# Kernel tuning notes

Measured on AMD Instinct MI355X. Metric: run time of the kernel, lower is better.

The kernel has to match this reference:

```python
import jax, jax.numpy as jnp
import numpy as np
import math

N_HEADS = 16

def _rope_tables(T, D, dtype):
    # inv_freq over even dims, emb = [freqs, freqs] -> [T, D]
    inv_freq = 1.0 / (10000.0 ** (jnp.arange(0, D, 2, dtype=jnp.float32) / D))
    freqs = jnp.arange(T, dtype=jnp.float32)[:, None] * inv_freq[None, :]  # [T, D/2]
    emb = jnp.concatenate([freqs, freqs], axis=-1)  # [T, D]
    return jnp.cos(emb).astype(dtype), jnp.sin(emb).astype(dtype)

def _rotate_half(x):
    d = x.shape[-1] // 2
    return jnp.concatenate([-x[..., d:], x[..., :d]], axis=-1)

def setup_inputs() -> dict:
    key = jax.random.key(0)
    ks = jax.random.split(key, 5)
    B, T, C = 2, 2048, 1024
    s = 1.0 / math.sqrt(C)
    return {
        "x": jax.random.normal(ks[0], (B, T, C), dtype=jnp.float32),
        "Wq": jax.random.normal(ks[1], (C, C), dtype=jnp.float32) * s,
        "Wk": jax.random.normal(ks[2], (C, C), dtype=jnp.float32) * s,
        "Wv": jax.random.normal(ks[3], (C, C), dtype=jnp.float32) * s,
        "Wo": jax.random.normal(ks[4], (C, C), dtype=jnp.float32) * s,
    }

def reference(x, Wq, Wk, Wv, Wo):
    B, T, C = x.shape
    H = N_HEADS
    D = C // H
    # QKV projections (torch Linear, bias=False: y = x @ W.T), split into heads
    def proj(W):
        return (x @ W.T).reshape(B, T, H, D).transpose(0, 2, 1, 3)  # [B,H,T,D]
    q, k, v = proj(Wq), proj(Wk), proj(Wv)
    # RoPE
    cos, sin = _rope_tables(T, D, x.dtype)  # [T,D] each, broadcast over B,H
    q = q * cos + _rotate_half(q) * sin
    k = k * cos + _rotate_half(k) * sin
    # scaled dot-product attention with causal mask
    scale = 1.0 / math.sqrt(D)
    attn = jnp.einsum('bhtd,bhsd->bhts', q, k) * scale  # [B,H,T,T]
    row = jnp.arange(T)[:, None]
    col = jnp.arange(T)[None, :]
    attn = jnp.where(col > row, -jnp.inf, attn)
    p = jax.nn.softmax(attn, axis=-1)
    out = jnp.einsum('bhts,bhsd->bhtd', p, v)  # [B,H,T,D]
    out = out.transpose(0, 2, 1, 3).reshape(B, T, C)
    return out @ Wo.T
```

## Files before the change

### kernel.cpp

```cpp
#include <hip/hip_runtime.h>
#include <hip/hip_bf16.h>


typedef __hip_bfloat16 bf16;
typedef __attribute__((ext_vector_type(8))) short bf16x8;
typedef __attribute__((ext_vector_type(4))) float f32x4;
typedef __attribute__((ext_vector_type(4))) short short4v;

#define MFMA16(a, b, c) __builtin_amdgcn_mfma_f32_16x16x32_bf16((a), (b), (c), 0, 0, 0)

constexpr int Bn = 2, Hn = 16, Tn = 2048, Dn = 64, Cn = 1024;
constexpr size_t NE = (size_t)Bn * Tn * Cn;
constexpr size_t WE = (size_t)Cn * Cn;
constexpr float QSCALE = 0.125f * 1.44269504088896f;

__device__ inline unsigned short bfbits(float x) {
    bf16 b = __float2bfloat16(x);
    return *(unsigned short*)&b;
}

__device__ inline bf16x8 pack8(f32x4 a, f32x4 b) {
    bf16x8 r;
#pragma unroll
    for (int i = 0; i < 4; ++i) r[i] = (short)bfbits(a[i]);
#pragma unroll
    for (int i = 0; i < 4; ++i) r[4 + i] = (short)bfbits(b[i]);
    return r;
}

__device__ inline void gl_lds16(const bf16* g, unsigned short* l) {
    __builtin_amdgcn_global_load_lds(
        (const __attribute__((address_space(1))) void*)g,
        (__attribute__((address_space(3))) void*)l, 16, 0, 0);
}

__device__ inline void stage64(const bf16* gbase, int ld, unsigned short* lds,
                               int wave, int lane) {
#pragma unroll
    for (int j = 0; j < 2; ++j) {
        int p = j * 256 + wave * 64 + lane;
        int row = p >> 3, ch = (p & 7) ^ (row & 7);
        gl_lds16(gbase + (size_t)row * ld + ch * 8,
                 lds + (size_t)(j * 256 + wave * 64) * 8);
    }
}

__device__ inline bf16x8 ldsfrag(const unsigned short* base, int row, int ch) {
    return *(const bf16x8*)&base[row * 64 + ((ch ^ (row & 7)) * 8)];
}

__global__ __launch_bounds__(256) void convert_kernel(
    const float* __restrict__ x, const float* __restrict__ wq,
    const float* __restrict__ wk, const float* __restrict__ wv,
    const float* __restrict__ wo, bf16* __restrict__ dst)
{
    int blk = blockIdx.x;
    int lane = threadIdx.x & 63;
    int lx = lane & 15, quad = lane >> 4;
    const float* src;
    size_t doff;
    if (blk < 2048) {
        int frag = blk * 4 + (threadIdx.x >> 6);
        int mt = frag >> 5, kc = frag & 31;
        src = x + (size_t)(mt * 16 + lx) * Cn + kc * 32 + quad * 8;
        doff = (size_t)frag * 512 + lane * 8;
    } else {
        int w = (blk - 2048) >> 9, b = (blk - 2048) & 511;
        const float* s4[4] = {wq, wk, wv, wo};
        int frag = b * 4 + (threadIdx.x >> 6);
        int nb = frag >> 5, kc = frag & 31;
        src = s4[w] + (size_t)(nb * 16 + lx) * Cn + kc * 32 + quad * 8;
        doff = NE + (size_t)w * WE + (size_t)frag * 512 + lane * 8;
    }
    f32x4 a = *(const f32x4*)(src);
    f32x4 b2 = *(const f32x4*)(src + 4);
    *(bf16x8*)(dst + doff) = pack8(a, b2);
}

__global__ __launch_bounds__(256) void gemm_qkv_kernel(
    const bf16* __restrict__ Xf, const bf16* __restrict__ Wbase,
    bf16* __restrict__ Qo, bf16* __restrict__ Ko, bf16* __restrict__ Vo)
{
    const int bm = blockIdx.x, bn = blockIdx.y, wsel = blockIdx.z;
    const bf16* W = Wbase + (size_t)wsel * WE;
    const int tid  = threadIdx.x;
    const int wave = tid >> 6, lane = tid & 63;
    const int lx   = lane & 15, quad = lane >> 4;
    const int wm = wave >> 1, wn = wave & 1;

    const int mt0 = bm * 8 + wm * 4;
    const int nb0 = bn * 8 + wn * 4;
    const bf16* afrag = Xf + (size_t)mt0 * 32 * 512 + (size_t)lane * 8;
    const bf16* wfrag = W + (size_t)nb0 * 32 * 512 + (size_t)lane * 8;

    f32x4 acc[4][4] = {};
    bf16x8 acur[4], bcur[4], anxt[4], bnxt[4];
#pragma unroll
    for (int i = 0; i < 4; ++i) {
        acur[i] = *(const bf16x8*)(afrag + (size_t)i * 32 * 512);
        bcur[i] = *(const bf16x8*)(wfrag + (size_t)i * 32 * 512);
    }
    for (int kc = 0; kc < 32; ++kc) {
        if (kc < 31) {
#pragma unroll
            for (int i = 0; i < 4; ++i) {
                anxt[i] = *(const bf16x8*)(afrag + ((size_t)i * 32 + kc + 1) * 512);
                bnxt[i] = *(const bf16x8*)(wfrag + ((size_t)i * 32 + kc + 1) * 512);
            }
        }
#pragma unroll
        for (int mt = 0; mt < 4; ++mt)
#pragma unroll
            for (int nt = 0; nt < 4; ++nt)
                acc[mt][nt] = MFMA16(acur[mt], bcur[nt], acc[mt][nt]);
#pragma unroll
        for (int i = 0; i < 4; ++i) { acur[i] = anxt[i]; bcur[i] = bnxt[i]; }
    }

    const int h = bn * 2 + wn;
    if (wsel <= 1) {
#pragma unroll
        for (int mt = 0; mt < 4; ++mt)
#pragma unroll
            for (int r = 0; r < 4; ++r) {
                int mg = bm * 128 + wm * 64 + mt * 16 + quad * 4 + r;
                int t  = mg & (Tn - 1);
#pragma unroll
                for (int nt = 0; nt < 2; ++nt) {
                    int d = nt * 16 + lx;
                    float ang = (float)t * __expf(-(float)d * 0.2878231366f);
                    float c, s;
                    __sincosf(ang, &s, &c);
                    float a0 = acc[mt][nt][r], a1 = acc[mt][nt + 2][r];
                    acc[mt][nt][r]     = a0 * c - a1 * s;
                    acc[mt][nt + 2][r] = a1 * c + a0 * s;
                }
            }
    }

#pragma unroll
    for (int mt = 0; mt < 4; ++mt) {
        int mg0 = bm * 128 + wm * 64 + mt * 16 + quad * 4;
        int b = mg0 >> 11, t0 = mg0 & (Tn - 1);
        if (wsel == 0) {
#pragma unroll
            for (int nt = 0; nt < 4; ++nt)
#pragma unroll
                for (int r = 0; r < 4; ++r) {
                    int d = nt * 16 + lx;
                    Qo[((size_t)(b * Hn + h) * Tn + t0 + r) * Dn + d] =
                        __float2bfloat16(acc[mt][nt][r] * QSCALE);
                }
        } else if (wsel == 1) {
#pragma unroll
            for (int nt = 0; nt < 4; ++nt)
#pragma unroll
                for (int r = 0; r < 4; ++r) {
                    int d = nt * 16 + lx;
                    Ko[((size_t)(b * Hn + h) * Tn + t0 + r) * Dn + d] =
                        __float2bfloat16(acc[mt][nt][r]);
                }
        } else {
#pragma unroll
            for (int nt = 0; nt < 4; ++nt) {
                int d = nt * 16 + lx;
                short4v pk;
#pragma unroll
                for (int r = 0; r < 4; ++r) pk[r] = (short)bfbits(acc[mt][nt][r]);
                *(short4v*)&Vo[((size_t)(b * Hn + h) * Dn + d) * Tn + t0] = pk;
            }
        }
    }
}

__global__ __launch_bounds__(256) void gemm_out_kernel(
    const bf16* __restrict__ Af, const bf16* __restrict__ W, float* __restrict__ Out)
{
    const int bm = blockIdx.x, bn = blockIdx.y;
    const int tid  = threadIdx.x;
    const int wave = tid >> 6, lane = tid & 63;
    const int lx   = lane & 15, quad = lane >> 4;
    const int wm = wave >> 1, wn = wave & 1;

    const int mt0 = bm * 8 + wm * 4;
    const int nb0 = bn * 4 + wn * 2;
    const bf16* afrag = Af + (size_t)mt0 * 32 * 512 + (size_t)lane * 8;
    const bf16* wfrag = W + (size_t)nb0 * 32 * 512 + (size_t)lane * 8;

    f32x4 acc[4][2] = {};
    bf16x8 acur[4], bcur[2], anxt[4], bnxt[2];
#pragma unroll
    for (int i = 0; i < 4; ++i)
        acur[i] = *(const bf16x8*)(afrag + (size_t)i * 32 * 512);
#pragma unroll
    for (int i = 0; i < 2; ++i)
        bcur[i] = *(const bf16x8*)(wfrag + (size_t)i * 32 * 512);
    for (int kc = 0; kc < 32; ++kc) {
        if (kc < 31) {
#pragma unroll
            for (int i = 0; i < 4; ++i)
                anxt[i] = *(const bf16x8*)(afrag + ((size_t)i * 32 + kc + 1) * 512);
#pragma unroll
            for (int i = 0; i < 2; ++i)
                bnxt[i] = *(const bf16x8*)(wfrag + ((size_t)i * 32 + kc + 1) * 512);
        }
#pragma unroll
        for (int mt = 0; mt < 4; ++mt)
#pragma unroll
            for (int nt = 0; nt < 2; ++nt)
                acc[mt][nt] = MFMA16(acur[mt], bcur[nt], acc[mt][nt]);
#pragma unroll
        for (int i = 0; i < 4; ++i) acur[i] = anxt[i];
#pragma unroll
        for (int i = 0; i < 2; ++i) bcur[i] = bnxt[i];
    }
#pragma unroll
    for (int mt = 0; mt < 4; ++mt)
#pragma unroll
        for (int nt = 0; nt < 2; ++nt)
#pragma unroll
            for (int r = 0; r < 4; ++r) {
                int mg = bm * 128 + wm * 64 + mt * 16 + quad * 4 + r;
                int ng = bn * 64 + wn * 32 + nt * 16 + lx;
                Out[(size_t)mg * Cn + ng] = acc[mt][nt][r];
            }
}

__global__ __launch_bounds__(256) void attn_kernel(
    const bf16* __restrict__ Q, const bf16* __restrict__ K,
    const bf16* __restrict__ Vt, bf16* __restrict__ O)
{
    __shared__ unsigned short Ks[64 * 64];
    __shared__ unsigned short Vs[64 * 64];
    __shared__ unsigned short Pl[4][16 * 72];
    const int f  = blockIdx.x;
    const int bh = (f & 7) * 4 + ((f >> 3) & 3);
    const int qb = 31 - (f >> 5);
    const int tid  = threadIdx.x;
    const int wave = tid >> 6, lane = tid & 63;
    const int lx   = lane & 15, quad = lane >> 4;

    const bf16* Qh = Q  + (size_t)bh * Tn * Dn;
    const bf16* Kh = K  + (size_t)bh * Tn * Dn;
    const bf16* Vh = Vt + (size_t)bh * Dn * Tn;
    unsigned short* pw = &Pl[wave][0];

    const int qrowA = qb * 64 + wave * 16 + lx;
    bf16x8 aq0 = *(const bf16x8*)(Qh + (size_t)qrowA * Dn + quad * 8);
    bf16x8 aq1 = *(const bf16x8*)(Qh + (size_t)qrowA * Dn + 32 + quad * 8);

    bf16x8 ones;
#pragma unroll
    for (int i = 0; i < 8; ++i) ones[i] = (short)0x3F80;

    f32x4 acc_o[4] = {};
    f32x4 acc_l = {};
    const int row_local = wave * 16 + quad * 4;

    for (int c = 0; c <= qb; ++c) {
        __syncthreads();
        stage64(Kh + (size_t)c * 64 * Dn, Dn, Ks, wave, lane);
        stage64(Vh + (size_t)c * 64, Tn, Vs, wave, lane);
        __syncthreads();
        f32x4 accs[4] = {};
#pragma unroll
        for (int nt = 0; nt < 4; ++nt) {
            int key = nt * 16 + lx;
            bf16x8 k0 = ldsfrag(Ks, key, quad);
            bf16x8 k1 = ldsfrag(Ks, key, quad + 4);
            accs[nt] = MFMA16(aq0, k0, accs[nt]);
            accs[nt] = MFMA16(aq1, k1, accs[nt]);
        }
        if (c < qb) {
#pragma unroll
            for (int nt = 0; nt < 4; ++nt)
#pragma unroll
                for (int r = 0; r < 4; ++r)
                    pw[(quad * 4 + r) * 72 + nt * 16 + lx] = bfbits(exp2f(accs[nt][r]));
        } else {
#pragma unroll
            for (int nt = 0; nt < 4; ++nt) {
                int keyl = nt * 16 + lx;
#pragma unroll
                for (int r = 0; r < 4; ++r) {
                    float p = (keyl > row_local + r) ? 0.0f : exp2f(accs[nt][r]);
                    pw[(quad * 4 + r) * 72 + nt * 16 + lx] = bfbits(p);
                }
            }
        }
        asm volatile("s_waitcnt lgkmcnt(0)" ::: "memory");
        bf16x8 ap0 = *(const bf16x8*)&pw[lx * 72 + quad * 8];
        bf16x8 ap1 = *(const bf16x8*)&pw[lx * 72 + 32 + quad * 8];
        acc_l = MFMA16(ap0, ones, acc_l);
        acc_l = MFMA16(ap1, ones, acc_l);
#pragma unroll
        for (int dt = 0; dt < 4; ++dt) {
            int d = dt * 16 + lx;
            bf16x8 v0 = ldsfrag(Vs, d, quad);
            bf16x8 v1 = ldsfrag(Vs, d, quad + 4);
            acc_o[dt] = MFMA16(ap0, v0, acc_o[dt]);
            acc_o[dt] = MFMA16(ap1, v1, acc_o[dt]);
        }
    }

    const int b = bh >> 4, h = bh & 15;
    const int mtile = b * 128 + qb * 4 + wave;
#pragma unroll
    for (int dt = 0; dt < 4; ++dt) {
        int ch = h * 64 + dt * 16 + lx;
        size_t base = ((size_t)mtile * 32 + (ch >> 5)) * 512
                    + (size_t)(((ch >> 3) & 3) * 16) * 8 + (ch & 7);
#pragma unroll
        for (int r = 0; r < 4; ++r) {
            float o = acc_o[dt][r] / acc_l[r];
            O[base + (size_t)(quad * 4 + r) * 8] = __float2bfloat16(o);
        }
    }
}

extern "C" void kernel_launch(void* const* d_in, const int* in_sizes, int n_in,
                              void* d_out, int out_size, void* d_ws, size_t ws_size,
                              hipStream_t stream)
{
    const float* x  = (const float*)d_in[0];
    const float* Wq = (const float*)d_in[1];
    const float* Wk = (const float*)d_in[2];
    const float* Wv = (const float*)d_in[3];
    const float* Wo = (const float*)d_in[4];
    float* out = (float*)d_out;

    bf16* ws = (bf16*)d_ws;
    bf16* Xf = ws;
    bf16* Wb = ws + NE;
    bf16* Qb = ws + NE + 4 * WE;
    bf16* Kb = Qb + NE;
    bf16* Vb = Kb + NE;
    bf16* Ab = Xf;

    convert_kernel<<<4096, 256, 0, stream>>>(x, Wq, Wk, Wv, Wo, ws);
    gemm_qkv_kernel<<<dim3(32, 8, 3), 256, 0, stream>>>(Xf, Wb, Qb, Kb, Vb);
    attn_kernel<<<1024, 256, 0, stream>>>(Qb, Kb, Vb, Ab);
    gemm_out_kernel<<<dim3(32, 16), 256, 0, stream>>>(Ab, Wb + 3 * WE, out);
}
```

Baseline: 176.2 us.

## Store K and V in MFMA fragment order and load attention operands directly from global

```diff
diff --git a/kernel.cpp b/kernel.cpp
--- a/kernel.cpp
+++ b/kernel.cpp
@@ -26,27 +26,6 @@
 #pragma unroll
     for (int i = 0; i < 4; ++i) r[4 + i] = (short)bfbits(b[i]);
     return r;
-}
-
-__device__ inline void gl_lds16(const bf16* g, unsigned short* l) {
-    __builtin_amdgcn_global_load_lds(
-        (const __attribute__((address_space(1))) void*)g,
-        (__attribute__((address_space(3))) void*)l, 16, 0, 0);
-}
-
-__device__ inline void stage64(const bf16* gbase, int ld, unsigned short* lds,
-                               int wave, int lane) {
-#pragma unroll
-    for (int j = 0; j < 2; ++j) {
-        int p = j * 256 + wave * 64 + lane;
-        int row = p >> 3, ch = (p & 7) ^ (row & 7);
-        gl_lds16(gbase + (size_t)row * ld + ch * 8,
-                 lds + (size_t)(j * 256 + wave * 64) * 8);
-    }
-}
-
-__device__ inline bf16x8 ldsfrag(const unsigned short* base, int row, int ch) {
-    return *(const bf16x8*)&base[row * 64 + ((ch ^ (row & 7)) * 8)];
 }
 
 __global__ __launch_bounds__(256) void convert_kernel(
@@ -141,33 +120,39 @@
 #pragma unroll
     for (int mt = 0; mt < 4; ++mt) {
         int mg0 = bm * 128 + wm * 64 + mt * 16 + quad * 4;
-        int b = mg0 >> 11, t0 = mg0 & (Tn - 1);
+        int b = mg0 >> 11, tlo = mg0 & (Tn - 1);
         if (wsel == 0) {
 #pragma unroll
             for (int nt = 0; nt < 4; ++nt)
 #pragma unroll
                 for (int r = 0; r < 4; ++r) {
                     int d = nt * 16 + lx;
-                    Qo[((size_t)(b * Hn + h) * Tn + t0 + r) * Dn + d] =
+                    Qo[((size_t)(b * Hn + h) * Tn + tlo + r) * Dn + d] =
                         __float2bfloat16(acc[mt][nt][r] * QSCALE);
                 }
         } else if (wsel == 1) {
-#pragma unroll
-            for (int nt = 0; nt < 4; ++nt)
-#pragma unroll
-                for (int r = 0; r < 4; ++r) {
-                    int d = nt * 16 + lx;
-                    Ko[((size_t)(b * Hn + h) * Tn + t0 + r) * Dn + d] =
-                        __float2bfloat16(acc[mt][nt][r]);
-                }
+            bf16* Kf = Ko + (size_t)(b * Hn + h) * Tn * Dn;
+            int c = tlo >> 6, ntk = (tlo >> 4) & 3;
+#pragma unroll
+            for (int nt = 0; nt < 4; ++nt) {
+                size_t base = ((size_t)(c * 4 + ntk) * 2 + (nt >> 1)) * 512
+                            + (size_t)((nt & 1) * 2 + (lx >> 3)) * 128
+                            + (size_t)(tlo & 15) * 8 + (lx & 7);
+#pragma unroll
+                for (int r = 0; r < 4; ++r)
+                    Kf[base + (size_t)r * 8] = __float2bfloat16(acc[mt][nt][r]);
+            }
         } else {
+            bf16* Vf = Vo + (size_t)(b * Hn + h) * Tn * Dn;
+            int c = tlo >> 6, ksv = (tlo >> 5) & 1;
+            int qv = (tlo >> 3) & 3, pos0 = tlo & 7;
 #pragma unroll
             for (int nt = 0; nt < 4; ++nt) {
-                int d = nt * 16 + lx;
                 short4v pk;
 #pragma unroll
                 for (int r = 0; r < 4; ++r) pk[r] = (short)bfbits(acc[mt][nt][r]);
-                *(short4v*)&Vo[((size_t)(b * Hn + h) * Dn + d) * Tn + t0] = pk;
+                *(short4v*)&Vf[((size_t)(c * 8 + nt * 2 + ksv)) * 512
+                               + (size_t)qv * 128 + (size_t)lx * 8 + pos0] = pk;
             }
         }
     }
@@ -230,8 +215,6 @@
     const bf16* __restrict__ Q, const bf16* __restrict__ K,
     const bf16* __restrict__ Vt, bf16* __restrict__ O)
 {
-    __shared__ unsigned short Ks[64 * 64];
-    __shared__ unsigned short Vs[64 * 64];
     __shared__ unsigned short Pl[4][16 * 72];
     const int f  = blockIdx.x;
     const int bh = (f & 7) * 4 + ((f >> 3) & 3);
@@ -242,7 +225,7 @@
 
     const bf16* Qh = Q  + (size_t)bh * Tn * Dn;
     const bf16* Kh = K  + (size_t)bh * Tn * Dn;
-    const bf16* Vh = Vt + (size_t)bh * Dn * Tn;
+    const bf16* Vh = Vt + (size_t)bh * Tn * Dn;
     unsigned short* pw = &Pl[wave][0];
 
     const int qrowA = qb * 64 + wave * 16 + lx;
@@ -258,18 +241,21 @@
     const int row_local = wave * 16 + quad * 4;
 
     for (int c = 0; c <= qb; ++c) {
-        __syncthreads();
-        stage64(Kh + (size_t)c * 64 * Dn, Dn, Ks, wave, lane);
-        stage64(Vh + (size_t)c * 64, Tn, Vs, wave, lane);
-        __syncthreads();
+        const bf16* kc = Kh + (size_t)c * 4096 + (size_t)lane * 8;
+        const bf16* vc = Vh + (size_t)c * 4096 + (size_t)lane * 8;
         f32x4 accs[4] = {};
 #pragma unroll
         for (int nt = 0; nt < 4; ++nt) {
-            int key = nt * 16 + lx;
-            bf16x8 k0 = ldsfrag(Ks, key, quad);
-            bf16x8 k1 = ldsfrag(Ks, key, quad + 4);
+            bf16x8 k0 = *(const bf16x8*)(kc + (size_t)(nt * 2) * 512);
+            bf16x8 k1 = *(const bf16x8*)(kc + (size_t)(nt * 2 + 1) * 512);
             accs[nt] = MFMA16(aq0, k0, accs[nt]);
             accs[nt] = MFMA16(aq1, k1, accs[nt]);
+        }
+        bf16x8 vf0[4], vf1[4];
+#pragma unroll
+        for (int dt = 0; dt < 4; ++dt) {
+            vf0[dt] = *(const bf16x8*)(vc + (size_t)(dt * 2) * 512);
+            vf1[dt] = *(const bf16x8*)(vc + (size_t)(dt * 2 + 1) * 512);
         }
         if (c < qb) {
 #pragma unroll
@@ -295,11 +281,8 @@
         acc_l = MFMA16(ap1, ones, acc_l);
 #pragma unroll
         for (int dt = 0; dt < 4; ++dt) {
-            int d = dt * 16 + lx;
-            bf16x8 v0 = ldsfrag(Vs, d, quad);
-            bf16x8 v1 = ldsfrag(Vs, d, quad + 4);
-            acc_o[dt] = MFMA16(ap0, v0, acc_o[dt]);
-            acc_o[dt] = MFMA16(ap1, v1, acc_o[dt]);
+            acc_o[dt] = MFMA16(ap0, vf0[dt], acc_o[dt]);
+            acc_o[dt] = MFMA16(ap1, vf1[dt], acc_o[dt]);
         }
     }
 
```

Result: no change. 179.0 us (+1.6%).
